# Performance work log

Hardware: AMD Instinct MI355X
Metric: run time of the kernel (lower is better)

Reference implementation:

```python
import jax, jax.numpy as jnp
import numpy as np

B, S, E, CS, NC, H = 4, 2048, 1024, 16, 8, 16
D = E + CS            # d_model = 1040
DH = D // H           # head_dim = 65
DFF = 4 * E           # forward_expansion * embed_size


def setup_inputs() -> dict:
    key = jax.random.key(0)
    ks = jax.random.split(key, 20)
    s = 0.02  # init scale for weights
    f32 = jnp.float32
    return {
        'x': jax.random.normal(ks[0], (B, S, E), f32),
        'conditioning': jax.random.uniform(ks[1], (B, S, CS), f32),
        # attention params (torch Linear convention: W is [out, in])
        'Wq': jax.random.normal(ks[2], (D, D), f32) * s,
        'bq': jnp.zeros((D,), f32),
        'Wv': jax.random.normal(ks[3], (D, D), f32) * s,
        'bv': jnp.zeros((D,), f32),
        'Wk': jax.random.normal(ks[4], (NC, D, D), f32) * s,  # stacked per-class key projections
        'bk': jnp.zeros((NC, D), f32),
        'Wo': jax.random.normal(ks[5], (D, D), f32) * s,
        'bo': jnp.zeros((D,), f32),
        # layernorms
        'g1': jnp.ones((E,), f32), 'bn1': jnp.zeros((E,), f32),
        'g2': jnp.ones((E,), f32), 'bn2': jnp.zeros((E,), f32),
        # feed-forward
        'Wf1': jax.random.normal(ks[6], (DFF, E), f32) * s,
        'bf1': jnp.zeros((DFF,), f32),
        'Wf2': jax.random.normal(ks[7], (E, DFF), f32) * s,
        'bf2': jnp.zeros((E,), f32),
    }


def _layernorm(x, g, b, eps=1e-5):
    m = jnp.mean(x, axis=-1, keepdims=True)
    v = jnp.mean(jnp.square(x - m), axis=-1, keepdims=True)
    return (x - m) * jax.lax.rsqrt(v + eps) * g + b


def reference(x, conditioning, Wq, bq, Wv, bv, Wk, bk, Wo, bo,
              g1, bn1, g2, bn2, Wf1, bf1, Wf2, bf2):
    # dropout is identity (eval mode)
    xn = _layernorm(x, g1, bn1)                       # [B,S,E]
    xc = jnp.concatenate([xn, conditioning], axis=-1)  # [B,S,D]

    q = (xc @ Wq.T + bq).reshape(B, S, H, DH).transpose(0, 2, 1, 3)  # [B,H,S,DH]
    v = (xc @ Wv.T + bv).reshape(B, S, H, DH).transpose(0, 2, 1, 3)

    # per-class keys: [B,C,S,D], then weighted-sum by conditioning[:,:,:NC]
    keys = jnp.einsum('bsd,cod->bcso', xc, Wk) + bk[None, :, None, :]
    w = conditioning[:, :, :NC]                        # [B,S,C]
    k = jnp.einsum('bsc,bcso->bso', w, keys)           # [B,S,D]
    k = k.reshape(B, S, H, DH).transpose(0, 2, 1, 3)   # [B,H,S,DH]

    scale = 1.0 / np.sqrt(DH).astype(np.float32)
    scores = jnp.einsum('bhqd,bhkd->bhqk', q, k) * scale
    attn = jax.nn.softmax(scores, axis=-1)
    o = jnp.einsum('bhqk,bhkd->bhqd', attn, v)
    o = o.transpose(0, 2, 1, 3).reshape(B, S, D)
    o = o @ Wo.T + bo

    h = xn + o[:, :, :E]                               # residual uses normed x
    ff = jnp.maximum(h @ Wf1.T + bf1, 0.0) @ Wf2.T + bf2
    return _layernorm(h + ff, g2, bn2)
```

## Files before the change

### kernel.cpp

```cpp
#include <hip/hip_runtime.h>
#include <hip/hip_bf16.h>
#include <math.h>

typedef __bf16 bf16;
typedef __bf16 v8bf __attribute__((ext_vector_type(8)));
typedef float v4f __attribute__((ext_vector_type(4)));

#define B_   4
#define S_   2048
#define E_   1024
#define CS_  16
#define NC_  8
#define H_   16
#define D_   1040
#define DH_  65
#define DFF_ 4096
#define M_   8192

__device__ __forceinline__ v4f mfma16(v8bf a, v8bf b, v4f c) {
    return __builtin_amdgcn_mfma_f32_16x16x32_bf16(a, b, c, 0, 0, 0);
}

__device__ __forceinline__ void async16(const bf16* g, bf16* l) {
    __builtin_amdgcn_global_load_lds(
        (const __attribute__((address_space(1))) unsigned int*)g,
        (__attribute__((address_space(3))) unsigned int*)l, 16, 0, 0);
}

__global__ __launch_bounds__(256) void k_cvt(const float* __restrict__ src,
                                             bf16* __restrict__ dst, int n) {
    int i = (blockIdx.x * 256 + threadIdx.x) * 4;
    if (i + 4 <= n) {
        float4 v = *(const float4*)(src + i);
        bf16 o[4] = {(bf16)v.x, (bf16)v.y, (bf16)v.z, (bf16)v.w};
        *(ushort4*)(dst + i) = *(const ushort4*)o;
    }
}

__global__ __launch_bounds__(256) void k_zero(uint4* __restrict__ p, int n4) {
    int i = blockIdx.x * 256 + threadIdx.x;
    uint4 z = {0u, 0u, 0u, 0u};
    if (i < n4) p[i] = z;
}

__global__ __launch_bounds__(256) void k_ln_concat(
    const float* __restrict__ x, const float* __restrict__ cond,
    const float* __restrict__ g, const float* __restrict__ bn,
    bf16* __restrict__ xc)
{
    int row = blockIdx.x;
    int t = threadIdx.x;
    const float* xr = x + (size_t)row * E_;
    float4 v = *(const float4*)(xr + t * 4);
    float s = v.x + v.y + v.z + v.w;
    float ss = v.x * v.x + v.y * v.y + v.z * v.z + v.w * v.w;
#pragma unroll
    for (int off = 32; off; off >>= 1) {
        s  += __shfl_down(s, off);
        ss += __shfl_down(ss, off);
    }
    __shared__ float red[8];
    int wid = t >> 6;
    if ((t & 63) == 0) { red[wid] = s; red[4 + wid] = ss; }
    __syncthreads();
    float stot  = red[0] + red[1] + red[2] + red[3];
    float sstot = red[4] + red[5] + red[6] + red[7];
    float mean = stot * (1.0f / E_);
    float var  = sstot * (1.0f / E_) - mean * mean;
    float rs = rsqrtf(var + 1e-5f);
    bf16* xcr = xc + (size_t)row * D_;
    float vv[4] = {v.x, v.y, v.z, v.w};
#pragma unroll
    for (int j = 0; j < 4; ++j) {
        int i = t * 4 + j;
        xcr[i] = (bf16)(((vv[j] - mean) * rs) * g[i] + bn[i]);
    }
    if (t < CS_) xcr[E_ + t] = (bf16)cond[(size_t)row * CS_ + t];
}

#define EP_QV  0
#define EP_K   1
#define EP_O   2
#define EP_FF1 3
#define EP_FF2 4

template<int EP>
__global__ __launch_bounds__(256) void k_gemm(
    const bf16* __restrict__ A, const bf16* __restrict__ Bm,
    const float* __restrict__ bias, const float* __restrict__ bias2,
    int M, int N, int K, int lda, int ldb, int nbn,
    bf16* __restrict__ Cb, float* __restrict__ Cf, int ldc,
    const bf16* __restrict__ res, int ldres,
    const float* __restrict__ condw, const float* __restrict__ bkp)
{
    __shared__ bf16 As[128][32];
    __shared__ bf16 Bs[128][32];
    int t = threadIdx.x;

    int pid = blockIdx.x;
    int nig = 8 * nbn;
    int gid = pid / nig;
    int rem = pid - gid * nig;
    int mi = gid * 8 + (rem & 7);
    int ni = rem >> 3;
    int m0 = mi << 7, n0 = ni << 7;

    int lane = t & 63, w = t >> 6;
    int wm = (w >> 1) * 64, wn = (w & 1) * 64;
    int lr = lane & 15, lq = lane >> 4;

    int row_i[2], seg_i[2];
#pragma unroll
    for (int i = 0; i < 2; ++i) { row_i[i] = (t + i * 256) >> 2; seg_i[i] = (t + i * 256) & 3; }

    v4f acc[4][4];
    v4f vzero = {0.f, 0.f, 0.f, 0.f};
#pragma unroll
    for (int mt = 0; mt < 4; ++mt)
#pragma unroll
        for (int nt = 0; nt < 4; ++nt) acc[mt][nt] = vzero;

    const int KF = K >> 5;
    const bool KR = (K & 31) != 0;
    const int CLOOP = (EP == EP_K) ? NC_ : 1;

    for (int c = 0; c < CLOOP; ++c) {
        const bf16* Bc = (EP == EP_K) ? (Bm + (size_t)c * D_ * D_) : Bm;
        float wsc[2];
        if constexpr (EP == EP_K) {
#pragma unroll
            for (int i = 0; i < 2; ++i) wsc[i] = condw[(size_t)(m0 + row_i[i]) * CS_ + c];
        }
        for (int kb = 0; kb < KF; ++kb) {
            int k0 = kb << 5;
            if constexpr (EP == EP_K) {
#pragma unroll
                for (int i = 0; i < 2; ++i) {
                    uint4 val = *(const uint4*)(A + (size_t)(m0 + row_i[i]) * lda + k0 + seg_i[i] * 8);
                    union { uint4 u; bf16 h[8]; } u8;
                    u8.u = val;
#pragma unroll
                    for (int j = 0; j < 8; ++j) u8.h[j] = (bf16)((float)u8.h[j] * wsc[i]);
                    *(uint4*)(&As[row_i[i]][seg_i[i] * 8]) = u8.u;
                }
            } else {
#pragma unroll
                for (int i = 0; i < 2; ++i)
                    async16(A + (size_t)(m0 + row_i[i]) * lda + k0 + seg_i[i] * 8,
                            &As[0][0] + (t + i * 256) * 8);
            }
#pragma unroll
            for (int i = 0; i < 2; ++i)
                async16(Bc + (size_t)(n0 + row_i[i]) * ldb + k0 + seg_i[i] * 8,
                        &Bs[0][0] + (t + i * 256) * 8);
            __syncthreads();
            v8bf af[4], bfr[4];
#pragma unroll
            for (int mt = 0; mt < 4; ++mt) af[mt]  = *(const v8bf*)(&As[wm + mt * 16 + lr][lq * 8]);
#pragma unroll
            for (int nt = 0; nt < 4; ++nt) bfr[nt] = *(const v8bf*)(&Bs[wn + nt * 16 + lr][lq * 8]);
#pragma unroll
            for (int mt = 0; mt < 4; ++mt)
#pragma unroll
                for (int nt = 0; nt < 4; ++nt)
                    acc[mt][nt] = mfma16(af[mt], bfr[nt], acc[mt][nt]);
            __syncthreads();
        }
        if (KR) {
            int k0 = KF << 5;
#pragma unroll
            for (int i = 0; i < 2; ++i) {
                int gk = k0 + seg_i[i] * 8;
                uint4 val = {0u, 0u, 0u, 0u};
                if (gk + 8 <= K) val = *(const uint4*)(A + (size_t)(m0 + row_i[i]) * lda + gk);
                if constexpr (EP == EP_K) {
                    union { uint4 u; bf16 h[8]; } u8;
                    u8.u = val;
#pragma unroll
                    for (int j = 0; j < 8; ++j) u8.h[j] = (bf16)((float)u8.h[j] * wsc[i]);
                    val = u8.u;
                }
                *(uint4*)(&As[row_i[i]][seg_i[i] * 8]) = val;
                uint4 bv = {0u, 0u, 0u, 0u};
                int gn = n0 + row_i[i];
                if (gn < N && gk + 8 <= K) bv = *(const uint4*)(Bc + (size_t)gn * ldb + gk);
                *(uint4*)(&Bs[row_i[i]][seg_i[i] * 8]) = bv;
            }
            __syncthreads();
            v8bf af[4], bfr[4];
#pragma unroll
            for (int mt = 0; mt < 4; ++mt) af[mt]  = *(const v8bf*)(&As[wm + mt * 16 + lr][lq * 8]);
#pragma unroll
            for (int nt = 0; nt < 4; ++nt) bfr[nt] = *(const v8bf*)(&Bs[wn + nt * 16 + lr][lq * 8]);
#pragma unroll
            for (int mt = 0; mt < 4; ++mt)
#pragma unroll
                for (int nt = 0; nt < 4; ++nt)
                    acc[mt][nt] = mfma16(af[mt], bfr[nt], acc[mt][nt]);
            __syncthreads();
        }
    }

#pragma unroll
    for (int mt = 0; mt < 4; ++mt) {
#pragma unroll
        for (int reg = 0; reg < 4; ++reg) {
            int grow = m0 + wm + mt * 16 + lq * 4 + reg;
#pragma unroll
            for (int nt = 0; nt < 4; ++nt) {
                int gcol = n0 + wn + nt * 16 + lr;
                float vacc = acc[mt][nt][reg];
                if constexpr (EP == EP_QV) {
                    if (gcol < D_) {
                        float o = (vacc + bias[gcol]) * 0.1789442960f;
                        int h = gcol / 65, d = gcol - h * 65;
                        int b = grow >> 11, s = grow & 2047;
                        Cb[(((size_t)(b * 16 + h)) * S_ + s) * 96 + d] = (bf16)o;
                    } else if (gcol < 2 * D_) {
                        int col = gcol - D_;
                        ((bf16*)res)[(size_t)grow * D_ + col] = (bf16)(vacc + bias2[col]);
                    }
                } else if constexpr (EP == EP_K) {
                    if (gcol < D_) {
                        float bb = 0.f;
#pragma unroll
                        for (int cc = 0; cc < NC_; ++cc)
                            bb += condw[(size_t)grow * CS_ + cc] * bkp[(size_t)cc * D_ + gcol];
                        float o = vacc + bb;
                        int h = gcol / 65, d = gcol - h * 65;
                        int b = grow >> 11, s = grow & 2047;
                        Cb[(((size_t)(b * 16 + h)) * S_ + s) * 96 + d] = (bf16)o;
                    }
                } else if constexpr (EP == EP_O) {
                    float o = vacc + bias[gcol] + (float)res[(size_t)grow * ldres + gcol];
                    Cb[(size_t)grow * ldc + gcol] = (bf16)o;
                } else if constexpr (EP == EP_FF1) {
                    float o = vacc + bias[gcol];
                    Cb[(size_t)grow * ldc + gcol] = (bf16)fmaxf(o, 0.f);
                } else {
                    Cf[(size_t)grow * ldc + gcol] =
                        vacc + bias[gcol] + (float)res[(size_t)grow * ldres + gcol];
                }
            }
        }
    }
}

__global__ __launch_bounds__(256) void k_transpose_v(
    const bf16* __restrict__ v, bf16* __restrict__ vt)
{
    int bh = blockIdx.y, s0 = blockIdx.x * 64;
    int b = bh >> 4, h = bh & 15;
    __shared__ bf16 tile[80][65];
#pragma unroll
    for (int i = 0; i < 20; ++i) {
        int idx = threadIdx.x + i * 256;
        int d = idx % 80, sl = idx / 80;
        bf16 val = (bf16)0.f;
        if (d < DH_) val = v[((size_t)b * S_ + s0 + sl) * D_ + h * DH_ + d];
        tile[d][sl] = val;
    }
    __syncthreads();
#pragma unroll
    for (int i = 0; i < 20; ++i) {
        int idx = threadIdx.x + i * 256;
        int sl = idx % 64, d = idx / 64;
        vt[((size_t)bh * 80 + d) * S_ + s0 + sl] = tile[d][sl];
    }
}

__global__ __launch_bounds__(256) void k_attn(
    const bf16* __restrict__ qp, const bf16* __restrict__ kp,
    const bf16* __restrict__ vt, bf16* __restrict__ o)
{
    int bh = blockIdx.y;
    int s0 = blockIdx.x * 64;
    int b = bh >> 4, h = bh & 15;
    int t = threadIdx.x, lane = t & 63, w = t >> 6;
// ... 88 lines not shown

#pragma unroll
        for (int nt = 0; nt < 5; ++nt)
#pragma unroll
            for (int r = 0; r < 4; ++r) o_acc[nt][r] *= alpha[r];

#pragma unroll
        for (int kt = 0; kt < 2; ++kt) {
            v8bf ap = *(const v8bf*)(&Ps[lr * 72 + kt * 32 + lq * 8]);
#pragma unroll
            for (int nt = 0; nt < 5; ++nt) {
                v8bf bv2 = *(const v8bf*)(&Vs[nt * 16 + lr][kt * 32 + lq * 8]);
                o_acc[nt] = mfma16(ap, bv2, o_acc[nt]);
            }
        }
        __syncthreads();
    }

    float inv[4];
#pragma unroll
    for (int r = 0; r < 4; ++r) inv[r] = 1.0f / l_r[r];
    int token = b * S_ + s0 + w * 16 + lq * 4;
#pragma unroll
    for (int nt = 0; nt < 5; ++nt) {
        int d = nt * 16 + lr;
        if (d < DH_) {
#pragma unroll
            for (int r = 0; r < 4; ++r)
                o[(size_t)(token + r) * D_ + h * DH_ + d] = (bf16)(o_acc[nt][r] * inv[r]);
        }
    }
}

__global__ __launch_bounds__(256) void k_ln_out(
    const float* __restrict__ z, const float* __restrict__ g,
    const float* __restrict__ bn, float* __restrict__ out)
{
    int row = blockIdx.x;
    int t = threadIdx.x;
    const float* zr = z + (size_t)row * E_;
    float4 v = *(const float4*)(zr + t * 4);
    float s = v.x + v.y + v.z + v.w;
    float ss = v.x * v.x + v.y * v.y + v.z * v.z + v.w * v.w;
#pragma unroll
    for (int off = 32; off; off >>= 1) {
        s  += __shfl_down(s, off);
        ss += __shfl_down(ss, off);
    }
    __shared__ float red[8];
    int wid = t >> 6;
    if ((t & 63) == 0) { red[wid] = s; red[4 + wid] = ss; }
    __syncthreads();
    float stot  = red[0] + red[1] + red[2] + red[3];
    float sstot = red[4] + red[5] + red[6] + red[7];
    float mean = stot * (1.0f / E_);
    float var  = sstot * (1.0f / E_) - mean * mean;
    float rs = rsqrtf(var + 1e-5f);
    float* outr = out + (size_t)row * E_;
    float vv[4] = {v.x, v.y, v.z, v.w};
#pragma unroll
    for (int j = 0; j < 4; ++j) {
        int i = t * 4 + j;
        outr[i] = ((vv[j] - mean) * rs) * g[i] + bn[i];
    }
}

extern "C" void kernel_launch(void* const* d_in, const int* in_sizes, int n_in,
                              void* d_out, int out_size, void* d_ws, size_t ws_size,
                              hipStream_t stream) {
    const float* x    = (const float*)d_in[0];
    const float* cond = (const float*)d_in[1];
    const float* Wq   = (const float*)d_in[2];
    const float* bq   = (const float*)d_in[3];
    const float* Wv   = (const float*)d_in[4];
    const float* bv   = (const float*)d_in[5];
    const float* Wk   = (const float*)d_in[6];
    const float* bk   = (const float*)d_in[7];
    const float* Wo   = (const float*)d_in[8];
    const float* bo   = (const float*)d_in[9];
    const float* g1   = (const float*)d_in[10];
    const float* bn1  = (const float*)d_in[11];
    const float* g2   = (const float*)d_in[12];
    const float* bn2  = (const float*)d_in[13];
    const float* Wf1  = (const float*)d_in[14];
    const float* bf1  = (const float*)d_in[15];
    const float* Wf2  = (const float*)d_in[16];
    const float* bf2  = (const float*)d_in[17];
    float* out = (float*)d_out;

    char* ws = (char*)d_ws;
    bf16* Wqv_b = (bf16*)(ws + 0);
    bf16* Wk_b  = (bf16*)(ws + 4526080);
    bf16* Wo_b  = (bf16*)(ws + 21831680);
    bf16* Wf1_b = (bf16*)(ws + 23994880);
    bf16* Wf2_b = (bf16*)(ws + 32383488);
    bf16*  xc  = (bf16*)(ws + 40772096);
    bf16*  ob  = (bf16*)(ws + 57811456);
    bf16*  vb  = (bf16*)(ws + 74850816);
    bf16*  hb  = (bf16*)(ws + 74850816);
    bf16*  qp  = (bf16*)(ws + 91890176);
    bf16*  kp  = (bf16*)(ws + 117056000);
    bf16*  vtb = (bf16*)(ws + 142221824);
    bf16*  ff1 = (bf16*)(ws + 91890176);
    float* zb  = (float*)(ws + 40772096);

    k_cvt<<<(1081600 / 4 + 255) / 256, 256, 0, stream>>>(Wq, Wqv_b, 1081600);
    k_cvt<<<(1081600 / 4 + 255) / 256, 256, 0, stream>>>(Wv, Wqv_b + 1081600, 1081600);
    k_cvt<<<(8652800 / 4 + 255) / 256, 256, 0, stream>>>(Wk, Wk_b, 8652800);
    k_cvt<<<(1081600 / 4 + 255) / 256, 256, 0, stream>>>(Wo, Wo_b, 1081600);
    k_cvt<<<(4194304 / 4 + 255) / 256, 256, 0, stream>>>(Wf1, Wf1_b, 4194304);
    k_cvt<<<(4194304 / 4 + 255) / 256, 256, 0, stream>>>(Wf2, Wf2_b, 4194304);

    k_ln_concat<<<M_, 256, 0, stream>>>(x, cond, g1, bn1, xc);

    k_zero<<<(4456448 + 255) / 256, 256, 0, stream>>>((uint4*)(ws + 91890176), 4456448);

    k_gemm<EP_QV><<<64 * 17, 256, 0, stream>>>(xc, Wqv_b, bq, bv, M_, 2 * D_, D_, D_, D_, 17,
                                               qp, (float*)vb, 0, (const bf16*)vb, 0, nullptr, nullptr);
    k_gemm<EP_K><<<64 * 9, 256, 0, stream>>>(xc, Wk_b, nullptr, nullptr, M_, D_, D_, D_, D_, 9,
                                             kp, nullptr, 0, nullptr, 0, cond, bk);

    k_transpose_v<<<dim3(S_ / 64, 64), 256, 0, stream>>>(vb, vtb);
    k_attn<<<dim3(S_ / 64, 64), 256, 0, stream>>>(qp, kp, vtb, ob);

    k_gemm<EP_O><<<64 * 8, 256, 0, stream>>>(ob, Wo_b, bo, nullptr, M_, E_, D_, D_, D_, 8,
                                             hb, nullptr, E_, xc, D_, nullptr, nullptr);
    k_gemm<EP_FF1><<<64 * 32, 256, 0, stream>>>(hb, Wf1_b, bf1, nullptr, M_, DFF_, E_, E_, E_, 32,
                                                ff1, nullptr, DFF_, nullptr, 0, nullptr, nullptr);
    k_gemm<EP_FF2><<<64 * 8, 256, 0, stream>>>(ff1, Wf2_b, bf2, nullptr, M_, E_, DFF_, DFF_, DFF_, 8,
                                               nullptr, zb, E_, hb, E_, nullptr, nullptr);

    k_ln_out<<<M_, 256, 0, stream>>>(zb, g2, bn2, out);
}
```

Baseline: 1.095 ms.

## Split-K the K, O and FF2 GEMMs into two halves with combine kernels

The per-class key GEMM, the output projection and the FF2 GEMM each had only 512-576 tiles, which underfills the GPU. Each is now split along K (or over the class loop) into two partial products stored in bf16, with 1152 or 1024 blocks in total. Separate combine kernels add the partials with the bias and residual, and for FF2 the combine is fused into the final layernorm. The full pad-zeroing pass is also reduced to zeroing only the pad columns of q and k. The cost is extra partial-buffer traffic, extra launches, and the precision loss from rounding partials to bf16.

```diff
diff --git a/kernel.cpp b/kernel.cpp
--- a/kernel.cpp
+++ b/kernel.cpp
@@ -37,10 +37,13 @@
     }
 }
 
-__global__ __launch_bounds__(256) void k_zero(uint4* __restrict__ p, int n4) {
+__global__ __launch_bounds__(256) void k_zero_pads(bf16* __restrict__ qp,
+                                                   bf16* __restrict__ kp) {
     int i = blockIdx.x * 256 + threadIdx.x;
+    int row = i >> 3, j = i & 7;
     uint4 z = {0u, 0u, 0u, 0u};
-    if (i < n4) p[i] = z;
+    bf16* base = (j < 4) ? qp : kp;
+    ((uint4*)(base + (size_t)row * 96 + 64))[j & 3] = z;
 }
 
 __global__ __launch_bounds__(256) void k_ln_concat(
@@ -79,19 +82,14 @@
 }
 
 #define EP_QV  0
-#define EP_K   1
-#define EP_O   2
-#define EP_FF1 3
-#define EP_FF2 4
+#define EP_FF1 1
 
 template<int EP>
 __global__ __launch_bounds__(256) void k_gemm(
     const bf16* __restrict__ A, const bf16* __restrict__ Bm,
     const float* __restrict__ bias, const float* __restrict__ bias2,
     int M, int N, int K, int lda, int ldb, int nbn,
-    bf16* __restrict__ Cb, float* __restrict__ Cf, int ldc,
-    const bf16* __restrict__ res, int ldres,
-    const float* __restrict__ condw, const float* __restrict__ bkp)
+    bf16* __restrict__ Cb, int ldc, bf16* __restrict__ Cb2)
 {
     __shared__ bf16 As[128][32];
     __shared__ bf16 Bs[128][32];
@@ -122,83 +120,54 @@
 
     const int KF = K >> 5;
     const bool KR = (K & 31) != 0;
-    const int CLOOP = (EP == EP_K) ? NC_ : 1;
-
-    for (int c = 0; c < CLOOP; ++c) {
-        const bf16* Bc = (EP == EP_K) ? (Bm + (size_t)c * D_ * D_) : Bm;
-        float wsc[2];
-        if constexpr (EP == EP_K) {
-#pragma unroll
-            for (int i = 0; i < 2; ++i) wsc[i] = condw[(size_t)(m0 + row_i[i]) * CS_ + c];
-        }
-        for (int kb = 0; kb < KF; ++kb) {
-            int k0 = kb << 5;
-            if constexpr (EP == EP_K) {
-#pragma unroll
-                for (int i = 0; i < 2; ++i) {
-                    uint4 val = *(const uint4*)(A + (size_t)(m0 + row_i[i]) * lda + k0 + seg_i[i] * 8);
-                    union { uint4 u; bf16 h[8]; } u8;
-                    u8.u = val;
-#pragma unroll
-                    for (int j = 0; j < 8; ++j) u8.h[j] = (bf16)((float)u8.h[j] * wsc[i]);
-                    *(uint4*)(&As[row_i[i]][seg_i[i] * 8]) = u8.u;
-                }
-            } else {
-#pragma unroll
-                for (int i = 0; i < 2; ++i)
-                    async16(A + (size_t)(m0 + row_i[i]) * lda + k0 + seg_i[i] * 8,
-                            &As[0][0] + (t + i * 256) * 8);
-            }
-#pragma unroll
-            for (int i = 0; i < 2; ++i)
-                async16(Bc + (size_t)(n0 + row_i[i]) * ldb + k0 + seg_i[i] * 8,
-                        &Bs[0][0] + (t + i * 256) * 8);
-            __syncthreads();
-            v8bf af[4], bfr[4];
-#pragma unroll
-            for (int mt = 0; mt < 4; ++mt) af[mt]  = *(const v8bf*)(&As[wm + mt * 16 + lr][lq * 8]);
-#pragma unroll
-            for (int nt = 0; nt < 4; ++nt) bfr[nt] = *(const v8bf*)(&Bs[wn + nt * 16 + lr][lq * 8]);
-#pragma unroll
-            for (int mt = 0; mt < 4; ++mt)
-#pragma unroll
-                for (int nt = 0; nt < 4; ++nt)
-                    acc[mt][nt] = mfma16(af[mt], bfr[nt], acc[mt][nt]);
-            __syncthreads();
-        }
-        if (KR) {
-            int k0 = KF << 5;
-#pragma unroll
-            for (int i = 0; i < 2; ++i) {
-                int gk = k0 + seg_i[i] * 8;
-                uint4 val = {0u, 0u, 0u, 0u};
-                if (gk + 8 <= K) val = *(const uint4*)(A + (size_t)(m0 + row_i[i]) * lda + gk);
-                if constexpr (EP == EP_K) {
-                    union { uint4 u; bf16 h[8]; } u8;
-                    u8.u = val;
-#pragma unroll
-                    for (int j = 0; j < 8; ++j) u8.h[j] = (bf16)((float)u8.h[j] * wsc[i]);
-                    val = u8.u;
-                }
-                *(uint4*)(&As[row_i[i]][seg_i[i] * 8]) = val;
-                uint4 bv = {0u, 0u, 0u, 0u};
-                int gn = n0 + row_i[i];
-                if (gn < N && gk + 8 <= K) bv = *(const uint4*)(Bc + (size_t)gn * ldb + gk);
-                *(uint4*)(&Bs[row_i[i]][seg_i[i] * 8]) = bv;
-            }
-            __syncthreads();
-            v8bf af[4], bfr[4];
-#pragma unroll
-            for (int mt = 0; mt < 4; ++mt) af[mt]  = *(const v8bf*)(&As[wm + mt * 16 + lr][lq * 8]);
-#pragma unroll
-            for (int nt = 0; nt < 4; ++nt) bfr[nt] = *(const v8bf*)(&Bs[wn + nt * 16 + lr][lq * 8]);
-#pragma unroll
-            for (int mt = 0; mt < 4; ++mt)
-#pragma unroll
-                for (int nt = 0; nt < 4; ++nt)
-                    acc[mt][nt] = mfma16(af[mt], bfr[nt], acc[mt][nt]);
-            __syncthreads();
-        }
+
+    for (int kb = 0; kb < KF; ++kb) {
+        int k0 = kb << 5;
+#pragma unroll
+        for (int i = 0; i < 2; ++i) {
+            async16(A + (size_t)(m0 + row_i[i]) * lda + k0 + seg_i[i] * 8,
+                    &As[0][0] + (t + i * 256) * 8);
+            async16(Bm + (size_t)(n0 + row_i[i]) * ldb + k0 + seg_i[i] * 8,
+                    &Bs[0][0] + (t + i * 256) * 8);
+        }
+        __syncthreads();
+        v8bf af[4], bfr[4];
+#pragma unroll
+        for (int mt = 0; mt < 4; ++mt) af[mt]  = *(const v8bf*)(&As[wm + mt * 16 + lr][lq * 8]);
+#pragma unroll
+        for (int nt = 0; nt < 4; ++nt) bfr[nt] = *(const v8bf*)(&Bs[wn + nt * 16 + lr][lq * 8]);
+#pragma unroll
+        for (int mt = 0; mt < 4; ++mt)
+#pragma unroll
+            for (int nt = 0; nt < 4; ++nt)
+                acc[mt][nt] = mfma16(af[mt], bfr[nt], acc[mt][nt]);
+        __syncthreads();
+    }
+    if (KR) {
+        int k0 = KF << 5;
+#pragma unroll
+        for (int i = 0; i < 2; ++i) {
+            int gk = k0 + seg_i[i] * 8;
+            uint4 val = {0u, 0u, 0u, 0u};
+            if (gk + 8 <= K) val = *(const uint4*)(A + (size_t)(m0 + row_i[i]) * lda + gk);
+            *(uint4*)(&As[row_i[i]][seg_i[i] * 8]) = val;
+            uint4 bv = {0u, 0u, 0u, 0u};
+            int gn = n0 + row_i[i];
+            if (gn < N && gk + 8 <= K) bv = *(const uint4*)(Bm + (size_t)gn * ldb + gk);
+            *(uint4*)(&Bs[row_i[i]][seg_i[i] * 8]) = bv;
+        }
+        __syncthreads();
+        v8bf af[4], bfr[4];
+#pragma unroll
+        for (int mt = 0; mt < 4; ++mt) af[mt]  = *(const v8bf*)(&As[wm + mt * 16 + lr][lq * 8]);
+#pragma unroll
+        for (int nt = 0; nt < 4; ++nt) bfr[nt] = *(const v8bf*)(&Bs[wn + nt * 16 + lr][lq * 8]);
+#pragma unroll
+        for (int mt = 0; mt < 4; ++mt)
+#pragma unroll
+            for (int nt = 0; nt < 4; ++nt)
+                acc[mt][nt] = mfma16(af[mt], bfr[nt], acc[mt][nt]);
+        __syncthreads();
     }
 
 #pragma unroll
@@ -218,32 +187,242 @@
                         Cb[(((size_t)(b * 16 + h)) * S_ + s) * 96 + d] = (bf16)o;
                     } else if (gcol < 2 * D_) {
                         int col = gcol - D_;
-                        ((bf16*)res)[(size_t)grow * D_ + col] = (bf16)(vacc + bias2[col]);
+                        Cb2[(size_t)grow * D_ + col] = (bf16)(vacc + bias2[col]);
                     }
-                } else if constexpr (EP == EP_K) {
-                    if (gcol < D_) {
-                        float bb = 0.f;
-#pragma unroll
-                        for (int cc = 0; cc < NC_; ++cc)
-                            bb += condw[(size_t)grow * CS_ + cc] * bkp[(size_t)cc * D_ + gcol];
-                        float o = vacc + bb;
-                        int h = gcol / 65, d = gcol - h * 65;
-                        int b = grow >> 11, s = grow & 2047;
-                        Cb[(((size_t)(b * 16 + h)) * S_ + s) * 96 + d] = (bf16)o;
-                    }
-                } else if constexpr (EP == EP_O) {
-                    float o = vacc + bias[gcol] + (float)res[(size_t)grow * ldres + gcol];
-                    Cb[(size_t)grow * ldc + gcol] = (bf16)o;
-                } else if constexpr (EP == EP_FF1) {
+                } else {
                     float o = vacc + bias[gcol];
                     Cb[(size_t)grow * ldc + gcol] = (bf16)fmaxf(o, 0.f);
-                } else {
-                    Cf[(size_t)grow * ldc + gcol] =
-                        vacc + bias[gcol] + (float)res[(size_t)grow * ldres + gcol];
                 }
             }
         }
     }
+}
+
+__global__ __launch_bounds__(256) void k_gemm_kp(
+    const bf16* __restrict__ A, const bf16* __restrict__ Bm,
+    const float* __restrict__ condw,
+    bf16* __restrict__ P0, bf16* __restrict__ P1)
+{
+    __shared__ bf16 As[128][32];
+    __shared__ bf16 Bs[128][32];
+    int t = threadIdx.x;
+
+    int sp = blockIdx.x / 576;
+    int pid = blockIdx.x - sp * 576;
+    int nig = 72;
+    int gid = pid / nig;
+    int rem = pid - gid * nig;
+    int mi = gid * 8 + (rem & 7);
+    int ni = rem >> 3;
+    int m0 = mi << 7, n0 = ni << 7;
+    bf16* Pout = sp ? P1 : P0;
+    int c0 = sp * 4;
+
+    int lane = t & 63, w = t >> 6;
+    int wm = (w >> 1) * 64, wn = (w & 1) * 64;
+    int lr = lane & 15, lq = lane >> 4;
+
+    int row_i[2], seg_i[2];
+#pragma unroll
+    for (int i = 0; i < 2; ++i) { row_i[i] = (t + i * 256) >> 2; seg_i[i] = (t + i * 256) & 3; }
+
+    v4f acc[4][4];
+    v4f vzero = {0.f, 0.f, 0.f, 0.f};
+#pragma unroll
+    for (int mt = 0; mt < 4; ++mt)
+#pragma unroll
+        for (int nt = 0; nt < 4; ++nt) acc[mt][nt] = vzero;
+
+    for (int cc = 0; cc < 4; ++cc) {
+        int c = c0 + cc;
+        const bf16* Bc = Bm + (size_t)c * D_ * D_;
+        float wsc[2];
+#pragma unroll
+        for (int i = 0; i < 2; ++i) wsc[i] = condw[(size_t)(m0 + row_i[i]) * CS_ + c];
+        for (int kb = 0; kb < 33; ++kb) {
+            int k0 = kb << 5;
+#pragma unroll
+            for (int i = 0; i < 2; ++i) {
+                int gk = k0 + seg_i[i] * 8;
+                uint4 val = {0u, 0u, 0u, 0u};
+                if (gk + 8 <= D_) val = *(const uint4*)(A + (size_t)(m0 + row_i[i]) * D_ + gk);
+                union { uint4 u; bf16 h[8]; } u8;
+                u8.u = val;
+#pragma unroll
+                for (int j = 0; j < 8; ++j) u8.h[j] = (bf16)((float)u8.h[j] * wsc[i]);
+                *(uint4*)(&As[row_i[i]][seg_i[i] * 8]) = u8.u;
+            }
+            if (kb < 32) {
+#pragma unroll
+                for (int i = 0; i < 2; ++i)
+                    async16(Bc + (size_t)(n0 + row_i[i]) * D_ + k0 + seg_i[i] * 8,
+                            &Bs[0][0] + (t + i * 256) * 8);
+            } else {
+#pragma unroll
+                for (int i = 0; i < 2; ++i) {
+                    int gk = k0 + seg_i[i] * 8;
+                    uint4 bv = {0u, 0u, 0u, 0u};
+                    if (gk + 8 <= D_) bv = *(const uint4*)(Bc + (size_t)(n0 + row_i[i]) * D_ + gk);
+                    *(uint4*)(&Bs[row_i[i]][seg_i[i] * 8]) = bv;
+                }
+            }
+            __syncthreads();
+            v8bf af[4], bfr[4];
+#pragma unroll
+            for (int mt = 0; mt < 4; ++mt) af[mt]  = *(const v8bf*)(&As[wm + mt * 16 + lr][lq * 8]);
+#pragma unroll
+            for (int nt = 0; nt < 4; ++nt) bfr[nt] = *(const v8bf*)(&Bs[wn + nt * 16 + lr][lq * 8]);
+#pragma unroll
+            for (int mt = 0; mt < 4; ++mt)
+#pragma unroll
+                for (int nt = 0; nt < 4; ++nt)
+                    acc[mt][nt] = mfma16(af[mt], bfr[nt], acc[mt][nt]);
+            __syncthreads();
+        }
+    }
+
+#pragma unroll
+    for (int mt = 0; mt < 4; ++mt)
+#pragma unroll
+        for (int reg = 0; reg < 4; ++reg) {
+            int grow = m0 + wm + mt * 16 + lq * 4 + reg;
+#pragma unroll
+            for (int nt = 0; nt < 4; ++nt) {
+                int gcol = n0 + wn + nt * 16 + lr;
+                if (gcol < D_)
+                    Pout[(size_t)grow * D_ + gcol] = (bf16)acc[mt][nt][reg];
+            }
+        }
+}
+
+__global__ __launch_bounds__(256) void k_gemm_part(
+    const bf16* __restrict__ A, const bf16* __restrict__ Bm,
+    int N, int lda, int ldb, int nbn, int bps, int klen0, int klen1,
+    bf16* __restrict__ P0, bf16* __restrict__ P1, int ldc)
+{
+    __shared__ bf16 As[128][32];
+    __shared__ bf16 Bs[128][32];
+    int t = threadIdx.x;
+
+    int sp = blockIdx.x / bps;
+    int pid = blockIdx.x - sp * bps;
+    int nig = 8 * nbn;
+    int gid = pid / nig;
+    int rem = pid - gid * nig;
+    int mi = gid * 8 + (rem & 7);
+    int ni = rem >> 3;
+    int m0 = mi << 7, n0 = ni << 7;
+    int koff = sp ? klen0 : 0;
+    int K = sp ? klen1 : klen0;
+    bf16* Pout = sp ? P1 : P0;
+
+    int lane = t & 63, w = t >> 6;
+    int wm = (w >> 1) * 64, wn = (w & 1) * 64;
+    int lr = lane & 15, lq = lane >> 4;
+
+    int row_i[2], seg_i[2];
+#pragma unroll
+    for (int i = 0; i < 2; ++i) { row_i[i] = (t + i * 256) >> 2; seg_i[i] = (t + i * 256) & 3; }
+
+    v4f acc[4][4];
+    v4f vzero = {0.f, 0.f, 0.f, 0.f};
+#pragma unroll
+    for (int mt = 0; mt < 4; ++mt)
+#pragma unroll
+        for (int nt = 0; nt < 4; ++nt) acc[mt][nt] = vzero;
+
+    const int KF = K >> 5;
+    const bool KR = (K & 31) != 0;
+
+    for (int kb = 0; kb < KF; ++kb) {
+        int k0 = koff + (kb << 5);
+#pragma unroll
+        for (int i = 0; i < 2; ++i) {
+            async16(A + (size_t)(m0 + row_i[i]) * lda + k0 + seg_i[i] * 8,
+                    &As[0][0] + (t + i * 256) * 8);
+            async16(Bm + (size_t)(n0 + row_i[i]) * ldb + k0 + seg_i[i] * 8,
+                    &Bs[0][0] + (t + i * 256) * 8);
+        }
+        __syncthreads();
+        v8bf af[4], bfr[4];
+#pragma unroll
+        for (int mt = 0; mt < 4; ++mt) af[mt]  = *(const v8bf*)(&As[wm + mt * 16 + lr][lq * 8]);
+#pragma unroll
+        for (int nt = 0; nt < 4; ++nt) bfr[nt] = *(const v8bf*)(&Bs[wn + nt * 16 + lr][lq * 8]);
+#pragma unroll
+        for (int mt = 0; mt < 4; ++mt)
+#pragma unroll
+            for (int nt = 0; nt < 4; ++nt)
+                acc[mt][nt] = mfma16(af[mt], bfr[nt], acc[mt][nt]);
+        __syncthreads();
+    }
+    if (KR) {
+        int kl = KF << 5;
+#pragma unroll
+        for (int i = 0; i < 2; ++i) {
+            int gkl = kl + seg_i[i] * 8;
+            uint4 val = {0u, 0u, 0u, 0u};
+            uint4 bv  = {0u, 0u, 0u, 0u};
+            if (gkl + 8 <= K) {
+                val = *(const uint4*)(A + (size_t)(m0 + row_i[i]) * lda + koff + gkl);
+                bv  = *(const uint4*)(Bm + (size_t)(n0 + row_i[i]) * ldb + koff + gkl);
+            }
+            *(uint4*)(&As[row_i[i]][seg_i[i] * 8]) = val;
+            *(uint4*)(&Bs[row_i[i]][seg_i[i] * 8]) = bv;
+        }
+        __syncthreads();
+        v8bf af[4], bfr[4];
+#pragma unroll
+        for (int mt = 0; mt < 4; ++mt) af[mt]  = *(const v8bf*)(&As[wm + mt * 16 + lr][lq * 8]);
+#pragma unroll
+        for (int nt = 0; nt < 4; ++nt) bfr[nt] = *(const v8bf*)(&Bs[wn + nt * 16 + lr][lq * 8]);
+#pragma unroll
+        for (int mt = 0; mt < 4; ++mt)
+#pragma unroll
+            for (int nt = 0; nt < 4; ++nt)
+                acc[mt][nt] = mfma16(af[mt], bfr[nt], acc[mt][nt]);
+        __syncthreads();
+    }
+
+#pragma unroll
+    for (int mt = 0; mt < 4; ++mt)
+#pragma unroll
+        for (int reg = 0; reg < 4; ++reg) {
+            int grow = m0 + wm + mt * 16 + lq * 4 + reg;
+#pragma unroll
+            for (int nt = 0; nt < 4; ++nt) {
+                int gcol = n0 + wn + nt * 16 + lr;
+                if (gcol < N)
+                    Pout[(size_t)grow * ldc + gcol] = (bf16)acc[mt][nt][reg];
+            }
+        }
+}
+
+__global__ __launch_bounds__(256) void k_comb_k(
+    const bf16* __restrict__ P0, const bf16* __restrict__ P1,
+    const float* __restrict__ condw, const float* __restrict__ bkp,
+    bf16* __restrict__ kp)
+{
+    int idx = blockIdx.x * 256 + threadIdx.x;
+    int m = idx / 1040, n = idx - m * 1040;
+    float v = (float)P0[idx] + (float)P1[idx];
+#pragma unroll
+    for (int c = 0; c < NC_; ++c)
+        v += condw[(size_t)m * CS_ + c] * bkp[(size_t)c * D_ + n];
+    int h = n / 65, d = n - h * 65;
+    int b = m >> 11, s = m & 2047;
+    kp[(((size_t)(b * 16 + h)) * S_ + s) * 96 + d] = (bf16)v;
+}
+
+__global__ __launch_bounds__(256) void k_comb_o(
+    const bf16* __restrict__ P0, const bf16* __restrict__ P1,
+    const float* __restrict__ bo, const bf16* __restrict__ xc,
+    bf16* __restrict__ hb)
+{
+    int idx = blockIdx.x * 256 + threadIdx.x;
+    int m = idx >> 10, n = idx & 1023;
+    float v = (float)P0[idx] + (float)P1[idx] + bo[n] + (float)xc[(size_t)m * D_ + n];
+    hb[idx] = (bf16)v;
 }
 
 __global__ __launch_bounds__(256) void k_transpose_v(
@@ -398,16 +577,25 @@
     }
 }
 
-__global__ __launch_bounds__(256) void k_ln_out(
-    const float* __restrict__ z, const float* __restrict__ g,
-    const float* __restrict__ bn, float* __restrict__ out)
+__global__ __launch_bounds__(256) void k_ln_out2(
+    const bf16* __restrict__ P0, const bf16* __restrict__ P1,
+    const bf16* __restrict__ hb, const float* __restrict__ bf2,
+    const float* __restrict__ g, const float* __restrict__ bn,
+    float* __restrict__ out)
 {
     int row = blockIdx.x;
     int t = threadIdx.x;
-    const float* zr = z + (size_t)row * E_;
-    float4 v = *(const float4*)(zr + t * 4);
-    float s = v.x + v.y + v.z + v.w;
-    float ss = v.x * v.x + v.y * v.y + v.z * v.z + v.w * v.w;
+    size_t base = (size_t)row * E_ + t * 4;
+    union { ushort4 u; bf16 h[4]; } a, bpp, c;
+    a.u   = *(const ushort4*)(P0 + base);
+    bpp.u = *(const ushort4*)(P1 + base);
+    c.u   = *(const ushort4*)(hb + base);
+    float vv[4];
+#pragma unroll
+    for (int j = 0; j < 4; ++j)
+        vv[j] = (float)a.h[j] + (float)bpp.h[j] + bf2[t * 4 + j] + (float)c.h[j];
+    float s = vv[0] + vv[1] + vv[2] + vv[3];
+    float ss = vv[0] * vv[0] + vv[1] * vv[1] + vv[2] * vv[2] + vv[3] * vv[3];
 #pragma unroll
     for (int off = 32; off; off >>= 1) {
         s  += __shfl_down(s, off);
@@ -423,7 +611,6 @@
     float var  = sstot * (1.0f / E_) - mean * mean;
     float rs = rsqrtf(var + 1e-5f);
     float* outr = out + (size_t)row * E_;
-    float vv[4] = {v.x, v.y, v.z, v.w};
 #pragma unroll
     for (int j = 0; j < 4; ++j) {
         int i = t * 4 + j;
@@ -444,10 +631,10 @@
     const float* bk   = (const float*)d_in[7];
     const float* Wo   = (const float*)d_in[8];
     const float* bo   = (const float*)d_in[9];
+    const float* g2   = (const float*)d_in[12];
+    const float* bn2  = (const float*)d_in[13];
     const float* g1   = (const float*)d_in[10];
     const float* bn1  = (const float*)d_in[11];
-    const float* g2   = (const float*)d_in[12];
-    const float* bn2  = (const float*)d_in[13];
     const float* Wf1  = (const float*)d_in[14];
     const float* bf1  = (const float*)d_in[15];
     const float* Wf2  = (const float*)d_in[16];
@@ -468,7 +655,12 @@
     bf16*  kp  = (bf16*)(ws + 117056000);
     bf16*  vtb = (bf16*)(ws + 142221824);
     bf16*  ff1 = (bf16*)(ws + 91890176);
-    float* zb  = (float*)(ws + 40772096);
+    bf16* P0k = ob;
+    bf16* P1k = vtb;
+    bf16* P0o = qp;
+    bf16* P1o = kp;
+    bf16* P0f = (bf16*)(ws + 40772096);
+    bf16* P1f = (bf16*)(ws + 57549312);
 
     k_cvt<<<(1081600 / 4 + 255) / 256, 256, 0, stream>>>(Wq, Wqv_b, 1081600);
     k_cvt<<<(1081600 / 4 + 255) / 256, 256, 0, stream>>>(Wv, Wqv_b + 1081600, 1081600);
@@ -478,23 +670,24 @@
     k_cvt<<<(4194304 / 4 + 255) / 256, 256, 0, stream>>>(Wf2, Wf2_b, 4194304);
 
     k_ln_concat<<<M_, 256, 0, stream>>>(x, cond, g1, bn1, xc);
-
-    k_zero<<<(4456448 + 255) / 256, 256, 0, stream>>>((uint4*)(ws + 91890176), 4456448);
+    k_zero_pads<<<4096, 256, 0, stream>>>(qp, kp);
 
     k_gemm<EP_QV><<<64 * 17, 256, 0, stream>>>(xc, Wqv_b, bq, bv, M_, 2 * D_, D_, D_, D_, 17,
-                                               qp, (float*)vb, 0, (const bf16*)vb, 0, nullptr, nullptr);
-    k_gemm<EP_K><<<64 * 9, 256, 0, stream>>>(xc, Wk_b, nullptr, nullptr, M_, D_, D_, D_, D_, 9,
-                                             kp, nullptr, 0, nullptr, 0, cond, bk);
+                                               qp, 0, vb);
+    k_gemm_kp<<<1152, 256, 0, stream>>>(xc, Wk_b, cond, P0k, P1k);
+    k_comb_k<<<(M_ * D_) / 256, 256, 0, stream>>>(P0k, P1k, cond, bk, kp);
 
     k_transpose_v<<<dim3(S_ / 64, 64), 256, 0, stream>>>(vb, vtb);
     k_attn<<<dim3(S_ / 64, 64), 256, 0, stream>>>(qp, kp, vtb, ob);
 
-    k_gemm<EP_O><<<64 * 8, 256, 0, stream>>>(ob, Wo_b, bo, nullptr, M_, E_, D_, D_, D_, 8,
-                                             hb, nullptr, E_, xc, D_, nullptr, nullptr);
+    k_gemm_part<<<1024, 256, 0, stream>>>(ob, Wo_b, E_, D_, D_, 8, 512, 512, 528,
+                                          P0o, P1o, E_);
+    k_comb_o<<<(M_ * E_) / 256, 256, 0, stream>>>(P0o, P1o, bo, xc, hb);
+
     k_gemm<EP_FF1><<<64 * 32, 256, 0, stream>>>(hb, Wf1_b, bf1, nullptr, M_, DFF_, E_, E_, E_, 32,
-                                                ff1, nullptr, DFF_, nullptr, 0, nullptr, nullptr);
-    k_gemm<EP_FF2><<<64 * 8, 256, 0, stream>>>(ff1, Wf2_b, bf2, nullptr, M_, E_, DFF_, DFF_, DFF_, 8,
-                                               nullptr, zb, E_, hb, E_, nullptr, nullptr);
-
-    k_ln_out<<<M_, 256, 0, stream>>>(zb, g2, bn2, out);
-}
+                                                ff1, DFF_, nullptr);
+
+    k_gemm_part<<<1024, 256, 0, stream>>>(ff1, Wf2_b, E_, DFF_, DFF_, 8, 512, 2048, 2048,
+                                          P0f, P1f, E_);
+    k_ln_out2<<<M_, 256, 0, stream>>>(P0f, P1f, hb, bf2, g2, bn2, out);
+}
```

After: 1.138 ms. +3.9%, slower.

## Restructure per-class key projection as pre-scaled concatenated-K GEMMs

Applied to the files above, without the earlier changes.

The key projection used to loop over 8 classes inside one GEMM, scaling the A tile on the fly with synchronous loads. It now packs the stacked Wk into one wide [N, 8*1056] bf16 matrix and writes conditioning-scaled copies of xc into a [M, 4*1056] buffer. Two async-load GEMMs, each covering 4 classes, produce partial results. A combine kernel adds the partials and the class-weighted bias, and writes the head-split K layout. The full workspace zeroing is replaced by zeroing only the head-dim pad columns. The cost is a large extra buffer of scaled activations (written twice) plus extra kernel launches. The K-pad columns of the packed weights are never initialized and rely on zero A padding.

```diff
diff --git a/kernel.cpp b/kernel.cpp
--- a/kernel.cpp
+++ b/kernel.cpp
@@ -16,6 +16,9 @@
 #define DH_  65
 #define DFF_ 4096
 #define M_   8192
+#define KC_  1056
+#define KH_  (4 * KC_)
+#define KB2_ (8 * KC_)
 
 __device__ __forceinline__ v4f mfma16(v8bf a, v8bf b, v4f c) {
     return __builtin_amdgcn_mfma_f32_16x16x32_bf16(a, b, c, 0, 0, 0);
@@ -37,10 +40,56 @@
     }
 }
 
-__global__ __launch_bounds__(256) void k_zero(uint4* __restrict__ p, int n4) {
+__global__ __launch_bounds__(256) void k_build_bk(const float* __restrict__ Wk,
+                                                  bf16* __restrict__ Bp) {
+    int c = blockIdx.y;
+    int idx = blockIdx.x * 256 + threadIdx.x;
+    if (idx >= 1040 * 130) return;
+    int n = idx / 130, u = idx - n * 130;
+    const float* src = Wk + ((size_t)(c * D_ + n)) * D_ + u * 8;
+    float4 a = *(const float4*)src;
+    float4 b = *(const float4*)(src + 4);
+    bf16 o[8] = {(bf16)a.x, (bf16)a.y, (bf16)a.z, (bf16)a.w,
+                 (bf16)b.x, (bf16)b.y, (bf16)b.z, (bf16)b.w};
+    *(uint4*)(Bp + (size_t)n * KB2_ + c * KC_ + u * 8) = *(const uint4*)o;
+}
+
+__global__ __launch_bounds__(256) void k_scale_a(const bf16* __restrict__ xc,
+                                                 const float* __restrict__ cond,
+                                                 int coff, bf16* __restrict__ Ap) {
+    int idx = blockIdx.x * 256 + threadIdx.x;
+    int m = idx / 132, u = idx - m * 132;
+    int j = u * 8;
+    float4 w4 = *(const float4*)(cond + (size_t)m * CS_ + coff);
+    float wv[4] = {w4.x, w4.y, w4.z, w4.w};
+    bf16* dst = Ap + (size_t)m * KH_ + j;
+    if (j < D_) {
+        union { uint4 u4; bf16 h[8]; } src;
+        src.u4 = *(const uint4*)(xc + (size_t)m * D_ + j);
+        float xv[8];
+#pragma unroll
+        for (int e = 0; e < 8; ++e) xv[e] = (float)src.h[e];
+#pragma unroll
+        for (int cc = 0; cc < 4; ++cc) {
+            bf16 o[8];
+#pragma unroll
+            for (int e = 0; e < 8; ++e) o[e] = (bf16)(xv[e] * wv[cc]);
+            *(uint4*)(dst + cc * KC_) = *(const uint4*)o;
+        }
+    } else {
+        uint4 z = {0u, 0u, 0u, 0u};
+#pragma unroll
+        for (int cc = 0; cc < 4; ++cc) *(uint4*)(dst + cc * KC_) = z;
+    }
+}
+
+__global__ __launch_bounds__(256) void k_zero_pads(bf16* __restrict__ qp,
+                                                   bf16* __restrict__ kp) {
     int i = blockIdx.x * 256 + threadIdx.x;
+    int row = i >> 3, j = i & 7;
     uint4 z = {0u, 0u, 0u, 0u};
-    if (i < n4) p[i] = z;
+    bf16* base = (j < 4) ? qp : kp;
+    ((uint4*)(base + (size_t)row * 96 + 64))[j & 3] = z;
 }
 
 __global__ __launch_bounds__(256) void k_ln_concat(
@@ -78,11 +127,93 @@
     if (t < CS_) xcr[E_ + t] = (bf16)cond[(size_t)row * CS_ + t];
 }
 
+__global__ __launch_bounds__(256) void k_gemm_k2(
+    const bf16* __restrict__ A, const bf16* __restrict__ Bm,
+    int koffB, bf16* __restrict__ Pout)
+{
+    __shared__ bf16 As[128][32];
+    __shared__ bf16 Bs[128][32];
+    int t = threadIdx.x;
+
+    int pid = blockIdx.x;
+    int gid = pid / 72;
+    int rem = pid - gid * 72;
+    int mi = gid * 8 + (rem & 7);
+    int ni = rem >> 3;
+    int m0 = mi << 7, n0 = ni << 7;
+
+    int lane = t & 63, w = t >> 6;
+    int wm = (w >> 1) * 64, wn = (w & 1) * 64;
+    int lr = lane & 15, lq = lane >> 4;
+
+    int row_i[2], seg_i[2];
+#pragma unroll
+    for (int i = 0; i < 2; ++i) { row_i[i] = (t + i * 256) >> 2; seg_i[i] = (t + i * 256) & 3; }
+
+    v4f acc[4][4];
+    v4f vzero = {0.f, 0.f, 0.f, 0.f};
+#pragma unroll
+    for (int mt = 0; mt < 4; ++mt)
+#pragma unroll
+        for (int nt = 0; nt < 4; ++nt) acc[mt][nt] = vzero;
+
+    for (int kb = 0; kb < KH_ / 32; ++kb) {
+        int k0 = kb << 5;
+#pragma unroll
+        for (int i = 0; i < 2; ++i) {
+            async16(A + (size_t)(m0 + row_i[i]) * KH_ + k0 + seg_i[i] * 8,
+                    &As[0][0] + (t + i * 256) * 8);
+            async16(Bm + (size_t)(n0 + row_i[i]) * KB2_ + koffB + k0 + seg_i[i] * 8,
+                    &Bs[0][0] + (t + i * 256) * 8);
+        }
+        __syncthreads();
+        v8bf af[4], bfr[4];
+#pragma unroll
+        for (int mt = 0; mt < 4; ++mt) af[mt]  = *(const v8bf*)(&As[wm + mt * 16 + lr][lq * 8]);
+#pragma unroll
+        for (int nt = 0; nt < 4; ++nt) bfr[nt] = *(const v8bf*)(&Bs[wn + nt * 16 + lr][lq * 8]);
+#pragma unroll
+        for (int mt = 0; mt < 4; ++mt)
+#pragma unroll
+            for (int nt = 0; nt < 4; ++nt)
+                acc[mt][nt] = mfma16(af[mt], bfr[nt], acc[mt][nt]);
+        __syncthreads();
+    }
+
+#pragma unroll
+    for (int mt = 0; mt < 4; ++mt)
+#pragma unroll
+        for (int reg = 0; reg < 4; ++reg) {
+            int grow = m0 + wm + mt * 16 + lq * 4 + reg;
+#pragma unroll
+            for (int nt = 0; nt < 4; ++nt) {
+                int gcol = n0 + wn + nt * 16 + lr;
+                if (gcol < D_)
+                    Pout[(size_t)grow * D_ + gcol] = (bf16)acc[mt][nt][reg];
+            }
+        }
+}
+
+__global__ __launch_bounds__(256) void k_comb_k(
+    const bf16* __restrict__ P0, const bf16* __restrict__ P1,
+    const float* __restrict__ condw, const float* __restrict__ bkp,
+    bf16* __restrict__ kp)
+{
+    int idx = blockIdx.x * 256 + threadIdx.x;
+    int m = idx / 1040, n = idx - m * 1040;
+    float v = (float)P0[idx] + (float)P1[idx];
+#pragma unroll
+    for (int c = 0; c < NC_; ++c)
+        v += condw[(size_t)m * CS_ + c] * bkp[(size_t)c * D_ + n];
+    int h = n / 65, d = n - h * 65;
+    int b = m >> 11, s = m & 2047;
+    kp[(((size_t)(b * 16 + h)) * S_ + s) * 96 + d] = (bf16)v;
+}
+
 #define EP_QV  0
-#define EP_K   1
-#define EP_O   2
-#define EP_FF1 3
-#define EP_FF2 4
+#define EP_O   1
+#define EP_FF1 2
+#define EP_FF2 3
 
 template<int EP>
 __global__ __launch_bounds__(256) void k_gemm(
@@ -90,8 +221,7 @@
     const float* __restrict__ bias, const float* __restrict__ bias2,
     int M, int N, int K, int lda, int ldb, int nbn,
     bf16* __restrict__ Cb, float* __restrict__ Cf, int ldc,
-    const bf16* __restrict__ res, int ldres,
-    const float* __restrict__ condw, const float* __restrict__ bkp)
+    const bf16* __restrict__ res, int ldres, bf16* __restrict__ Cb2)
 {
     __shared__ bf16 As[128][32];
     __shared__ bf16 Bs[128][32];
@@ -122,83 +252,54 @@
 
     const int KF = K >> 5;
     const bool KR = (K & 31) != 0;
-    const int CLOOP = (EP == EP_K) ? NC_ : 1;
-
-    for (int c = 0; c < CLOOP; ++c) {
-        const bf16* Bc = (EP == EP_K) ? (Bm + (size_t)c * D_ * D_) : Bm;
-        float wsc[2];
-        if constexpr (EP == EP_K) {
-#pragma unroll
-            for (int i = 0; i < 2; ++i) wsc[i] = condw[(size_t)(m0 + row_i[i]) * CS_ + c];
-        }
-        for (int kb = 0; kb < KF; ++kb) {
-            int k0 = kb << 5;
-            if constexpr (EP == EP_K) {
-#pragma unroll
-                for (int i = 0; i < 2; ++i) {
-                    uint4 val = *(const uint4*)(A + (size_t)(m0 + row_i[i]) * lda + k0 + seg_i[i] * 8);
-                    union { uint4 u; bf16 h[8]; } u8;
-                    u8.u = val;
-#pragma unroll
-                    for (int j = 0; j < 8; ++j) u8.h[j] = (bf16)((float)u8.h[j] * wsc[i]);
-                    *(uint4*)(&As[row_i[i]][seg_i[i] * 8]) = u8.u;
-                }
-            } else {
-#pragma unroll
-                for (int i = 0; i < 2; ++i)
-                    async16(A + (size_t)(m0 + row_i[i]) * lda + k0 + seg_i[i] * 8,
-                            &As[0][0] + (t + i * 256) * 8);
-            }
-#pragma unroll
-            for (int i = 0; i < 2; ++i)
-                async16(Bc + (size_t)(n0 + row_i[i]) * ldb + k0 + seg_i[i] * 8,
-                        &Bs[0][0] + (t + i * 256) * 8);
-            __syncthreads();
-            v8bf af[4], bfr[4];
-#pragma unroll
-            for (int mt = 0; mt < 4; ++mt) af[mt]  = *(const v8bf*)(&As[wm + mt * 16 + lr][lq * 8]);
-#pragma unroll
-            for (int nt = 0; nt < 4; ++nt) bfr[nt] = *(const v8bf*)(&Bs[wn + nt * 16 + lr][lq * 8]);
-#pragma unroll
-            for (int mt = 0; mt < 4; ++mt)
-#pragma unroll
-                for (int nt = 0; nt < 4; ++nt)
-                    acc[mt][nt] = mfma16(af[mt], bfr[nt], acc[mt][nt]);
-            __syncthreads();
-        }
-        if (KR) {
-            int k0 = KF << 5;
-#pragma unroll
-            for (int i = 0; i < 2; ++i) {
-                int gk = k0 + seg_i[i] * 8;
-                uint4 val = {0u, 0u, 0u, 0u};
-                if (gk + 8 <= K) val = *(const uint4*)(A + (size_t)(m0 + row_i[i]) * lda + gk);
-                if constexpr (EP == EP_K) {
-                    union { uint4 u; bf16 h[8]; } u8;
-                    u8.u = val;
-#pragma unroll
-                    for (int j = 0; j < 8; ++j) u8.h[j] = (bf16)((float)u8.h[j] * wsc[i]);
-                    val = u8.u;
-                }
-                *(uint4*)(&As[row_i[i]][seg_i[i] * 8]) = val;
-                uint4 bv = {0u, 0u, 0u, 0u};
-                int gn = n0 + row_i[i];
-                if (gn < N && gk + 8 <= K) bv = *(const uint4*)(Bc + (size_t)gn * ldb + gk);
-                *(uint4*)(&Bs[row_i[i]][seg_i[i] * 8]) = bv;
-            }
-            __syncthreads();
-            v8bf af[4], bfr[4];
-#pragma unroll
-            for (int mt = 0; mt < 4; ++mt) af[mt]  = *(const v8bf*)(&As[wm + mt * 16 + lr][lq * 8]);
-#pragma unroll
-            for (int nt = 0; nt < 4; ++nt) bfr[nt] = *(const v8bf*)(&Bs[wn + nt * 16 + lr][lq * 8]);
-#pragma unroll
-            for (int mt = 0; mt < 4; ++mt)
-#pragma unroll
-                for (int nt = 0; nt < 4; ++nt)
-                    acc[mt][nt] = mfma16(af[mt], bfr[nt], acc[mt][nt]);
-            __syncthreads();
-        }
+
+    for (int kb = 0; kb < KF; ++kb) {
+        int k0 = kb << 5;
+#pragma unroll
+        for (int i = 0; i < 2; ++i) {
+            async16(A + (size_t)(m0 + row_i[i]) * lda + k0 + seg_i[i] * 8,
+                    &As[0][0] + (t + i * 256) * 8);
+            async16(Bm + (size_t)(n0 + row_i[i]) * ldb + k0 + seg_i[i] * 8,
+                    &Bs[0][0] + (t + i * 256) * 8);
+        }
+        __syncthreads();
+        v8bf af[4], bfr[4];
+#pragma unroll
+        for (int mt = 0; mt < 4; ++mt) af[mt]  = *(const v8bf*)(&As[wm + mt * 16 + lr][lq * 8]);
+#pragma unroll
+        for (int nt = 0; nt < 4; ++nt) bfr[nt] = *(const v8bf*)(&Bs[wn + nt * 16 + lr][lq * 8]);
+#pragma unroll
+        for (int mt = 0; mt < 4; ++mt)
+#pragma unroll
+            for (int nt = 0; nt < 4; ++nt)
+                acc[mt][nt] = mfma16(af[mt], bfr[nt], acc[mt][nt]);
+        __syncthreads();
+    }
+    if (KR) {
+        int k0 = KF << 5;
+#pragma unroll
+        for (int i = 0; i < 2; ++i) {
+            int gk = k0 + seg_i[i] * 8;
+            uint4 val = {0u, 0u, 0u, 0u};
+            if (gk + 8 <= K) val = *(const uint4*)(A + (size_t)(m0 + row_i[i]) * lda + gk);
+            *(uint4*)(&As[row_i[i]][seg_i[i] * 8]) = val;
+            uint4 bv = {0u, 0u, 0u, 0u};
+            int gn = n0 + row_i[i];
+            if (gn < N && gk + 8 <= K) bv = *(const uint4*)(Bm + (size_t)gn * ldb + gk);
+            *(uint4*)(&Bs[row_i[i]][seg_i[i] * 8]) = bv;
+        }
+        __syncthreads();
+        v8bf af[4], bfr[4];
+#pragma unroll
+        for (int mt = 0; mt < 4; ++mt) af[mt]  = *(const v8bf*)(&As[wm + mt * 16 + lr][lq * 8]);
+#pragma unroll
+        for (int nt = 0; nt < 4; ++nt) bfr[nt] = *(const v8bf*)(&Bs[wn + nt * 16 + lr][lq * 8]);
+#pragma unroll
+        for (int mt = 0; mt < 4; ++mt)
+#pragma unroll
+            for (int nt = 0; nt < 4; ++nt)
+                acc[mt][nt] = mfma16(af[mt], bfr[nt], acc[mt][nt]);
+        __syncthreads();
     }
 
 #pragma unroll
@@ -218,18 +319,7 @@
                         Cb[(((size_t)(b * 16 + h)) * S_ + s) * 96 + d] = (bf16)o;
                     } else if (gcol < 2 * D_) {
                         int col = gcol - D_;
-                        ((bf16*)res)[(size_t)grow * D_ + col] = (bf16)(vacc + bias2[col]);
-                    }
-                } else if constexpr (EP == EP_K) {
-                    if (gcol < D_) {
-                        float bb = 0.f;
-#pragma unroll
-                        for (int cc = 0; cc < NC_; ++cc)
-                            bb += condw[(size_t)grow * CS_ + cc] * bkp[(size_t)cc * D_ + gcol];
-                        float o = vacc + bb;
-                        int h = gcol / 65, d = gcol - h * 65;
-                        int b = grow >> 11, s = grow & 2047;
-                        Cb[(((size_t)(b * 16 + h)) * S_ + s) * 96 + d] = (bf16)o;
+                        Cb2[(size_t)grow * D_ + col] = (bf16)(vacc + bias2[col]);
                     }
                 } else if constexpr (EP == EP_O) {
                     float o = vacc + bias[gcol] + (float)res[(size_t)grow * ldres + gcol];
@@ -456,45 +546,52 @@
 
     char* ws = (char*)d_ws;
     bf16* Wqv_b = (bf16*)(ws + 0);
-    bf16* Wk_b  = (bf16*)(ws + 4526080);
-    bf16* Wo_b  = (bf16*)(ws + 21831680);
-    bf16* Wf1_b = (bf16*)(ws + 23994880);
-    bf16* Wf2_b = (bf16*)(ws + 32383488);
-    bf16*  xc  = (bf16*)(ws + 40772096);
-    bf16*  ob  = (bf16*)(ws + 57811456);
-    bf16*  vb  = (bf16*)(ws + 74850816);
-    bf16*  hb  = (bf16*)(ws + 74850816);
-    bf16*  qp  = (bf16*)(ws + 91890176);
-    bf16*  kp  = (bf16*)(ws + 117056000);
-    bf16*  vtb = (bf16*)(ws + 142221824);
-    bf16*  ff1 = (bf16*)(ws + 91890176);
-    float* zb  = (float*)(ws + 40772096);
+    bf16* Wo_b  = (bf16*)(ws + 4526080);
+    bf16* Wf1_b = (bf16*)(ws + 6656000);
+    bf16* Wf2_b = (bf16*)(ws + 15044608);
+    bf16*  xc   = (bf16*)(ws + 23433216);
+    bf16*  Bpk  = (bf16*)(ws + 40472576);
+    bf16*  Apk  = (bf16*)(ws + 59936768);
+    bf16*  P0k  = (bf16*)(ws + 129142784);
+    bf16*  P1k  = (bf16*)(ws + 146182144);
+    bf16*  qp   = (bf16*)(ws + 40472576);
+    bf16*  kp   = (bf16*)(ws + 65638400);
+    bf16*  vb   = (bf16*)(ws + 90804224);
+    bf16*  hb   = (bf16*)(ws + 90804224);
+    bf16*  vtb  = (bf16*)(ws + 107843584);
+    bf16*  ob   = (bf16*)(ws + 128815104);
+    bf16*  ff1  = (bf16*)(ws + 23433216);
+    float* zb   = (float*)(ws + 107843584);
 
     k_cvt<<<(1081600 / 4 + 255) / 256, 256, 0, stream>>>(Wq, Wqv_b, 1081600);
     k_cvt<<<(1081600 / 4 + 255) / 256, 256, 0, stream>>>(Wv, Wqv_b + 1081600, 1081600);
-    k_cvt<<<(8652800 / 4 + 255) / 256, 256, 0, stream>>>(Wk, Wk_b, 8652800);
-    k_cvt<<<(1081600 / 4 + 255) / 256, 256, 0, stream>>>(Wo, Wo_b, 1081600);
+    k_cvt<<<(1064960 / 4 + 255) / 256, 256, 0, stream>>>(Wo, Wo_b, 1064960);
     k_cvt<<<(4194304 / 4 + 255) / 256, 256, 0, stream>>>(Wf1, Wf1_b, 4194304);
     k_cvt<<<(4194304 / 4 + 255) / 256, 256, 0, stream>>>(Wf2, Wf2_b, 4194304);
 
     k_ln_concat<<<M_, 256, 0, stream>>>(x, cond, g1, bn1, xc);
 
-    k_zero<<<(4456448 + 255) / 256, 256, 0, stream>>>((uint4*)(ws + 91890176), 4456448);
+    k_build_bk<<<dim3((1040 * 130 + 255) / 256, 8), 256, 0, stream>>>(Wk, Bpk);
+    k_scale_a<<<(M_ * 132) / 256, 256, 0, stream>>>(xc, cond, 0, Apk);
+    k_gemm_k2<<<576, 256, 0, stream>>>(Apk, Bpk, 0, P0k);
+    k_scale_a<<<(M_ * 132) / 256, 256, 0, stream>>>(xc, cond, 4, Apk);
+    k_gemm_k2<<<576, 256, 0, stream>>>(Apk, Bpk, KH_, P1k);
+
+    k_zero_pads<<<4096, 256, 0, stream>>>(qp, kp);
+    k_comb_k<<<(M_ * D_) / 256, 256, 0, stream>>>(P0k, P1k, cond, bk, kp);
 
     k_gemm<EP_QV><<<64 * 17, 256, 0, stream>>>(xc, Wqv_b, bq, bv, M_, 2 * D_, D_, D_, D_, 17,
-                                               qp, (float*)vb, 0, (const bf16*)vb, 0, nullptr, nullptr);
-    k_gemm<EP_K><<<64 * 9, 256, 0, stream>>>(xc, Wk_b, nullptr, nullptr, M_, D_, D_, D_, D_, 9,
-                                             kp, nullptr, 0, nullptr, 0, cond, bk);
+                                               qp, nullptr, 0, nullptr, 0, vb);
 
     k_transpose_v<<<dim3(S_ / 64, 64), 256, 0, stream>>>(vb, vtb);
     k_attn<<<dim3(S_ / 64, 64), 256, 0, stream>>>(qp, kp, vtb, ob);
 
     k_gemm<EP_O><<<64 * 8, 256, 0, stream>>>(ob, Wo_b, bo, nullptr, M_, E_, D_, D_, D_, 8,
-                                             hb, nullptr, E_, xc, D_, nullptr, nullptr);
+                                             hb, nullptr, E_, xc, D_, nullptr);
     k_gemm<EP_FF1><<<64 * 32, 256, 0, stream>>>(hb, Wf1_b, bf1, nullptr, M_, DFF_, E_, E_, E_, 32,
-                                                ff1, nullptr, DFF_, nullptr, 0, nullptr, nullptr);
+                                                ff1, nullptr, DFF_, nullptr, 0, nullptr);
     k_gemm<EP_FF2><<<64 * 8, 256, 0, stream>>>(ff1, Wf2_b, bf2, nullptr, M_, E_, DFF_, DFF_, DFF_, 8,
-                                               nullptr, zb, E_, hb, E_, nullptr, nullptr);
+                                               nullptr, zb, E_, hb, E_, nullptr);
 
     k_ln_out<<<M_, 256, 0, stream>>>(zb, g2, bn2, out);
 }
```

After: 1.077 ms. About the same (-1.7%).
